# Kernel optimization log

Hardware: AMD Instinct MI355X
Metric: run time of the kernel (lower is better)

The kernel has to match this reference:

```python
import jax, jax.numpy as jnp
import numpy as np

T_TRACK = 256   # tracklets per graph
M_DET = 256     # detections per graph
N_NODES = T_TRACK + M_DET
D_IN = 512      # raw node feature dim (stand-in for CNN crop features)
D_EMB = 256     # node embedding dim
SLACK = 0.2
LAM = 5.0
SINK_ITERS = 8


def box_iou(a, b):
    # a, b: [E,4] boxes (x1,y1,x2,y2)
    ix1 = jnp.maximum(a[:, 0], b[:, 0])
    iy1 = jnp.maximum(a[:, 1], b[:, 1])
    ix2 = jnp.minimum(a[:, 2], b[:, 2])
    iy2 = jnp.minimum(a[:, 3], b[:, 3])
    inter = jnp.clip(ix2 - ix1, 0.0) * jnp.clip(iy2 - iy1, 0.0)
    area_a = (a[:, 2] - a[:, 0]) * (a[:, 3] - a[:, 1])
    area_b = (b[:, 2] - b[:, 0]) * (b[:, 3] - b[:, 1])
    return inter / (area_a + area_b - inter + 1e-8)


def mlp2(x, W1, b1, W2, b2):
    return jax.nn.sigmoid(jax.nn.relu(x @ W1 + b1) @ W2 + b2)


def setup_inputs() -> dict:
    key = jax.random.key(0)
    ks = jax.random.split(key, 16)
    x = jax.random.normal(ks[0], (N_NODES, D_IN), jnp.float32)
    coords = jax.random.uniform(ks[1], (N_NODES, 4), jnp.float32)
    # valid boxes: x1<x2, y1<y2
    c = jax.random.uniform(ks[2], (N_NODES, 2), jnp.float32) * 100.0
    wh = jax.random.uniform(ks[3], (N_NODES, 2), jnp.float32) * 20.0 + 1.0
    coords_original = jnp.concatenate([c, c + wh], axis=1)
    # bipartite edges: track i (node i) <-> det j (node T_TRACK+j), both directions;
    # first T*M edges satisfy src < dst (the half kept by the row<col mask)
    src = jnp.repeat(jnp.arange(T_TRACK, dtype=jnp.int32), M_DET)
    dst = jnp.tile(jnp.arange(M_DET, dtype=jnp.int32) + T_TRACK, T_TRACK)
    edge_index = jnp.stack([jnp.concatenate([src, dst]), jnp.concatenate([dst, src])])
    s = 0.05
    p = lambda k, shp: jax.random.normal(k, shp, jnp.float32) * s
    return dict(
        x=x, coords=coords, coords_original=coords_original, edge_index=edge_index,
        W_cnn=p(ks[4], (D_IN, D_EMB)), b_cnn=jnp.zeros((D_EMB,), jnp.float32),
        Wapp1=p(ks[5], (2 * D_EMB, 128)), bapp1=jnp.zeros((128,), jnp.float32),
        Wapp2=p(ks[6], (128, 1)), bapp2=jnp.zeros((1,), jnp.float32),
        Wg1=p(ks[7], (8, 32)), bg1=jnp.zeros((32,), jnp.float32),
        Wg2=p(ks[8], (32, 1)), bg2=jnp.zeros((1,), jnp.float32),
        Wa1=p(ks[9], (2, 8)), ba1=jnp.zeros((8,), jnp.float32),
        Wa2=p(ks[10], (8, 1)), ba2=jnp.zeros((1,), jnp.float32),
        Wo1=p(ks[11], (D_EMB, D_EMB)), Wo2=p(ks[12], (D_EMB, D_EMB)),
        bo=jnp.zeros((D_EMB,), jnp.float32),
        Wf1=p(ks[13], (2, 8)), bf1=jnp.zeros((8,), jnp.float32),
        Wf2=p(ks[14], (8, 1)), bf2=jnp.zeros((1,), jnp.float32),
    )


def reference(x, coords, coords_original, edge_index, W_cnn, b_cnn, Wapp1, bapp1, Wapp2, bapp2, Wg1, bg1, Wg2, bg2, Wa1, ba1, Wa2, ba2, Wo1, Wo2, bo, Wf1, bf1, Wf2, bf2):
    src, dst = edge_index[0], edge_index[1]
    h = jax.nn.relu(x @ W_cnn + b_cnn)                      # [N, D]
    # per-edge appearance / geometry affinities (vectorized over all edges)
    app = mlp2(jnp.concatenate([h[src], h[dst]], 1), Wapp1, bapp1, Wapp2, bapp2)[:, 0]
    geo = mlp2(jnp.concatenate([coords[src], coords[dst]], 1), Wg1, bg1, Wg2, bg2)[:, 0]
    iou = box_iou(coords_original[src], coords_original[dst])
    e = mlp2(jnp.stack([app, geo], -1), Wa1, ba1, Wa2, ba2)[:, 0]   # [E]
    # message passing (optimNet): edge-gated neighbor aggregation
    agg = jax.ops.segment_sum(e[:, None] * h[src], dst, num_segments=N_NODES)
    out = jax.nn.relu(h @ Wo1 + agg @ Wo2 + bo)             # [N, D]
    # directed (src < dst) half of the edges only
    eh = T_TRACK * M_DET
    a, b = out[src[:eh]], out[dst[:eh]]
    na = jnp.maximum(jnp.linalg.norm(a, axis=-1), 1e-6)
    nb = jnp.maximum(jnp.linalg.norm(b, axis=-1), 1e-6)
    cos = jnp.sum(a * b, -1) / (na * nb)
    score = mlp2(jnp.stack([cos, iou[:eh]], -1), Wf1, bf1, Wf2, bf2)[:, 0]
    # assignment matrix with slack row/col, Sinkhorn normalization
    slack_v = jnp.exp(jnp.float32(LAM * SLACK))
    mat = jnp.full((T_TRACK + 1, M_DET + 1), slack_v, jnp.float32)
    mat = mat.at[:T_TRACK, :M_DET].set(jnp.exp(LAM * score).reshape(T_TRACK, M_DET))
    for _ in range(SINK_ITERS):
        mat = mat / jnp.sum(mat, axis=1, keepdims=True)
        mat = mat / jnp.sum(mat, axis=0, keepdims=True)
    return mat[:T_TRACK, :M_DET].reshape(-1)                # [T*M]
```

## Files before the change

### kernel.cpp

```cpp
#include <hip/hip_runtime.h>
#include <math.h>


__device__ __forceinline__ float sigmoidf_(float x) { return 1.0f / (1.0f + expf(-x)); }

typedef _Float16 h2t __attribute__((ext_vector_type(2)));

__device__ __forceinline__ h2t pack2(float x, float y) {
  h2t r; r.x = (_Float16)x; r.y = (_Float16)y; return r;
}
__device__ __forceinline__ float fdot2f(h2t a, h2t b, float c) {
  return __builtin_amdgcn_fdot2(a, b, c, false);
}
template <int CTRL>
__device__ __forceinline__ float dpp_get(float x) {
  return __builtin_bit_cast(
      float, __builtin_amdgcn_mov_dpp(__builtin_bit_cast(int, x), CTRL, 0xF, 0xF, false));
}
template <int IMM>
__device__ __forceinline__ float swz_get(float x) {
  return __builtin_bit_cast(
      float, __builtin_amdgcn_ds_swizzle(__builtin_bit_cast(int, x), IMM));
}
__device__ __forceinline__ float allred16(float x) {
  x += dpp_get<0xB1>(x);
  x += dpp_get<0x4E>(x);
  x += dpp_get<0x141>(x);
  x += dpp_get<0x140>(x);
  return x;
}

__global__ __launch_bounds__(256)
void k1_h(const float* __restrict__ x, const float* __restrict__ Wc,
          const float* __restrict__ bc, float* __restrict__ h) {
  __shared__ __align__(16) float Ast[2][32][36];
  const int tid = threadIdx.x;
  const int tx = tid & 31, ty = tid >> 5;
  const int ar = tid >> 3, ac = (tid & 7) * 4;
  const int bm = blockIdx.y * 32, bn = blockIdx.x * 32;
  const float* __restrict__ Bp = Wc + bn + tx;
  const float* __restrict__ Ap = x + (bm + ar) * 512 + ac;
  float4 aA, aB;
  float bA[32], bB[32];
  float acc[4] = {0.f, 0.f, 0.f, 0.f};

#define G_LOAD(T, AREG, BARR, AP, BP, LDB)                             \
  {                                                                    \
    AREG = *reinterpret_cast<const float4*>((AP) + (T) * 32);          \
    _Pragma("unroll") for (int kk = 0; kk < 32; ++kk)                  \
        BARR[kk] = (BP)[((T) * 32 + kk) * (LDB)];                      \
  }
#define G_STORE(BUF, AREG)                                             \
  {                                                                    \
    Ast[BUF][ac + 0][ar] = AREG.x; Ast[BUF][ac + 1][ar] = AREG.y;      \
    Ast[BUF][ac + 2][ar] = AREG.z; Ast[BUF][ac + 3][ar] = AREG.w;      \
  }
#define G_COMP(BUF, BARR)                                              \
  {                                                                    \
    _Pragma("unroll") for (int kk = 0; kk < 32; ++kk) {                \
      const float4 a4 =                                                \
          *reinterpret_cast<const float4*>(&Ast[BUF][kk][4 * ty]);     \
      const float bv = BARR[kk];                                       \
      acc[0] = fmaf(a4.x, bv, acc[0]); acc[1] = fmaf(a4.y, bv, acc[1]);\
      acc[2] = fmaf(a4.z, bv, acc[2]); acc[3] = fmaf(a4.w, bv, acc[3]);\
    }                                                                  \
  }

  G_LOAD(0, aA, bA, Ap, Bp, 256);
  G_STORE(0, aA);
  __syncthreads();
  for (int t = 0; t < 16; t += 2) {
    G_LOAD(t + 1, aB, bB, Ap, Bp, 256);
    G_COMP(0, bA);
    G_STORE(1, aB);
    __syncthreads();
    if (t + 2 < 16) { G_LOAD(t + 2, aA, bA, Ap, Bp, 256); }
    G_COMP(1, bB);
    if (t + 2 < 16) { G_STORE(0, aA); }
    __syncthreads();
  }
  const float bias = bc[bn + tx];
#pragma unroll
  for (int i = 0; i < 4; ++i) {
    const float vv = acc[i] + bias;
    h[(bm + 4 * ty + i) * 256 + bn + tx] = vv > 0.f ? vv : 0.f;
  }
}

__global__ __launch_bounds__(256)
void k2_pqgw(const float* __restrict__ h, const float* __restrict__ W1,
             const float* __restrict__ b1, const float* __restrict__ Wo2,
             const float* __restrict__ Wo1, float* __restrict__ PQGW) {
  __shared__ __align__(16) float Ast[2][32][36];
  const int tid = threadIdx.x;
  const int tx = tid & 31, ty = tid >> 5;
  const int ar = tid >> 3, ac = (tid & 7) * 4;
  const int bm = blockIdx.y * 32, bn = blockIdx.x * 32;
  const int col = bn + tx;
  const float* __restrict__ Bp;
  int ldb;
  if (bn < 128)       { Bp = W1 + col; ldb = 128; }
  else if (bn < 256)  { Bp = W1 + 256 * 128 + (col - 128); ldb = 128; }
  else if (bn < 512)  { Bp = Wo2 + (col - 256); ldb = 256; }
  else                { Bp = Wo1 + (col - 512); ldb = 256; }
  const float* __restrict__ Ap = h + (bm + ar) * 256 + ac;
  float4 aA, aB;
  float bA[32], bB[32];
  float acc[4] = {0.f, 0.f, 0.f, 0.f};

  G_LOAD(0, aA, bA, Ap, Bp, ldb);
  G_STORE(0, aA);
  __syncthreads();
  for (int t = 0; t < 8; t += 2) {
    G_LOAD(t + 1, aB, bB, Ap, Bp, ldb);
    G_COMP(0, bA);
    G_STORE(1, aB);
    __syncthreads();
    if (t + 2 < 8) { G_LOAD(t + 2, aA, bA, Ap, Bp, ldb); }
    G_COMP(1, bB);
    if (t + 2 < 8) { G_STORE(0, aA); }
    __syncthreads();
  }
  const float bias = (bn < 128) ? b1[col] : 0.f;
#pragma unroll
  for (int i = 0; i < 4; ++i)
    PQGW[(bm + 4 * ty + i) * 768 + col] = acc[i] + bias;
}

__global__ __launch_bounds__(256)
void k3_edges(const float* __restrict__ PQGW, const float* __restrict__ coords,
              const float* __restrict__ co, const float* __restrict__ Wapp2,
              const float* __restrict__ bapp2, const float* __restrict__ Wg1,
              const float* __restrict__ bg1, const float* __restrict__ Wg2,
              const float* __restrict__ bg2, const float* __restrict__ Wa1,
              const float* __restrict__ ba1, const float* __restrict__ Wa2,
              const float* __restrict__ ba2, float* __restrict__ E1,
              float* __restrict__ E2, float* __restrict__ iou1) {
  __shared__ __align__(16) float Qs[256][33];
  __shared__ __align__(16) float sP[128], sQ[128], sW2[128];
  __shared__ __align__(16) float sWg1[256], sWg2[32], sGfix0[32], sGfix1[32];
  __shared__ float sWa1[16], sBa1[8], sWa2[8];
  const int tid = threadIdx.x;
  const int fr = blockIdx.x;
  if (tid < 128) {
    sP[tid] = PQGW[fr * 768 + tid];
    sQ[tid] = PQGW[fr * 768 + 128 + tid];
    sW2[tid] = Wapp2[tid];
  }
  sWg1[tid] = Wg1[tid];
  if (tid < 32) sWg2[tid] = Wg2[tid];
  if (tid < 16) sWa1[tid] = Wa1[tid];
  if (tid < 8) { sBa1[tid] = ba1[tid]; sWa2[tid] = Wa2[tid]; }
  __syncthreads();
  if (tid < 32) {
    float g0 = bg1[tid], g1 = g0;
#pragma unroll
    for (int q = 0; q < 4; ++q) {
      const float c = coords[fr * 4 + q];
      g0 = fmaf(c, sWg1[q * 32 + tid], g0);
      g1 = fmaf(c, sWg1[(4 + q) * 32 + tid], g1);
    }
    sGfix0[tid] = g0;
    sGfix1[tid] = g1;
  }
  __syncthreads();

  const int d = tid;
  const int srow = tid >> 3, scq = (tid & 7) * 4;
  float z0 = 0.f, z1 = 0.f;
  for (int c8 = 0; c8 < 8; ++c8) {
    const int j0 = c8 * 32;
#pragma unroll
    for (int k = 0; k < 8; ++k) {
      const int r = k * 32 + srow;
      const float4 v = *reinterpret_cast<const float4*>(
          &PQGW[(256 + r) * 768 + j0 + scq]);
      Qs[r][scq + 0] = v.x; Qs[r][scq + 1] = v.y;
      Qs[r][scq + 2] = v.z; Qs[r][scq + 3] = v.w;
    }
    __syncthreads();
    if (j0 < 128) {
#pragma unroll
      for (int j = 0; j < 32; ++j) {
        const int jj = j0 + j;
        float a = sQ[jj] + Qs[d][j];
        a = a > 0.f ? a : 0.f;
        z1 = fmaf(a, sW2[jj], z1);
      }
    } else {
#pragma unroll
      for (int j = 0; j < 32; ++j) {
        const int jj = j0 + j - 128;
        float a = sP[jj] + Qs[d][j];
        a = a > 0.f ? a : 0.f;
        z0 = fmaf(a, sW2[jj], z0);
      }
    }
    __syncthreads();
  }
  const float app0 = sigmoidf_(z0 + bapp2[0]);
  const float app1 = sigmoidf_(z1 + bapp2[0]);
  const float4 cp = *reinterpret_cast<const float4*>(coords + (256 + d) * 4);
  float gz0 = 0.f, gz1 = 0.f;
#pragma unroll
  for (int m = 0; m < 32; ++m) {
    float h0 = sGfix0[m];
    h0 = fmaf(cp.x, sWg1[(4 + 0) * 32 + m], h0);
    h0 = fmaf(cp.y, sWg1[(4 + 1) * 32 + m], h0);
    h0 = fmaf(cp.z, sWg1[(4 + 2) * 32 + m], h0);
    h0 = fmaf(cp.w, sWg1[(4 + 3) * 32 + m], h0);
    h0 = h0 > 0.f ? h0 : 0.f;
    gz0 = fmaf(h0, sWg2[m], gz0);
    float h1 = sGfix1[m];
    h1 = fmaf(cp.x, sWg1[0 * 32 + m], h1);
    h1 = fmaf(cp.y, sWg1[1 * 32 + m], h1);
    h1 = fmaf(cp.z, sWg1[2 * 32 + m], h1);
    h1 = fmaf(cp.w, sWg1[3 * 32 + m], h1);
    h1 = h1 > 0.f ? h1 : 0.f;
    gz1 = fmaf(h1, sWg2[m], gz1);
  }
  const float geo0 = sigmoidf_(gz0 + bg2[0]);
  const float geo1 = sigmoidf_(gz1 + bg2[0]);
  float ez0 = 0.f, ez1 = 0.f;
#pragma unroll
  for (int m = 0; m < 8; ++m) {
    float h0 = fmaf(app0, sWa1[m], fmaf(geo0, sWa1[8 + m], sBa1[m]));
    h0 = h0 > 0.f ? h0 : 0.f;
    ez0 = fmaf(h0, sWa2[m], ez0);
    float h1 = fmaf(app1, sWa1[m], fmaf(geo1, sWa1[8 + m], sBa1[m]));
    h1 = h1 > 0.f ? h1 : 0.f;
    ez1 = fmaf(h1, sWa2[m], ez1);
  }
  E1[fr * 256 + d] = sigmoidf_(ez0 + ba2[0]);
  E2[fr * 256 + d] = sigmoidf_(ez1 + ba2[0]);
  const float4 A4 = *reinterpret_cast<const float4*>(co + fr * 4);
  const float4 B4 = *reinterpret_cast<const float4*>(co + (256 + d) * 4);
  const float ix1 = fmaxf(A4.x, B4.x), iy1 = fmaxf(A4.y, B4.y);
  const float ix2 = fminf(A4.z, B4.z), iy2 = fminf(A4.w, B4.w);
  const float inter = fmaxf(ix2 - ix1, 0.f) * fmaxf(iy2 - iy1, 0.f);
  const float areaA = (A4.z - A4.x) * (A4.w - A4.y);
  const float areaB = (B4.z - B4.x) * (B4.w - B4.y);
  iou1[fr * 256 + d] = inter / (areaA + areaB - inter + 1e-8f);
}

__global__ __launch_bounds__(256)
void k5_out(const float* __restrict__ E1, const float* __restrict__ E2,
            const float* __restrict__ PQGW, const float* __restrict__ bo,
            float* __restrict__ outm) {
  __shared__ __align__(16) float Ast[2][32][36];
  const int tid = threadIdx.x;
  const int tx = tid & 31, ty = tid >> 5;
  const int ar = tid >> 3, ac = (tid & 7) * 4;
  const int bm = blockIdx.y * 32, bn = blockIdx.x * 32;
  const int col = bn + tx;
  const bool detrows = (bm >= 256);
  const float* __restrict__ Ap = detrows
      ? (E1 + ar * 256 + (bm - 256) + ac)
      : (E2 + (bm + ar) * 256 + ac);
  const int astride = detrows ? 256 : 1;
  const float* __restrict__ Bp = PQGW + (detrows ? 0 : 256 * 768) + 256 + col;
  float4 aA, aB;
  float bA[32], bB[32];
  float acc[4] = {0.f, 0.f, 0.f, 0.f};

#define K5_LOAD(T, AREG, BARR)                                         \
  {                                                                    \
    AREG = *reinterpret_cast<const float4*>(Ap + (T) * 32 * astride);  \
    _Pragma("unroll") for (int kk = 0; kk < 32; ++kk)                  \
        BARR[kk] = Bp[((T) * 32 + kk) * 768];                          \
  }
#define K5_STORE(BUF, AREG)                                            \
  {                                                                    \
    if (detrows) {                                                     \
      *reinterpret_cast<float4*>(&Ast[BUF][ar][ac]) = AREG;            \
    } else {                                                           \
      Ast[BUF][ac + 0][ar] = AREG.x; Ast[BUF][ac + 1][ar] = AREG.y;    \
      Ast[BUF][ac + 2][ar] = AREG.z; Ast[BUF][ac + 3][ar] = AREG.w;    \
    }                                                                  \
  }

  K5_LOAD(0, aA, bA);
  K5_STORE(0, aA);
  __syncthreads();
  for (int t = 0; t < 8; t += 2) {
    K5_LOAD(t + 1, aB, bB);
    G_COMP(0, bA);
    K5_STORE(1, aB);
    __syncthreads();
    if (t + 2 < 8) { K5_LOAD(t + 2, aA, bA); }
    G_COMP(1, bB);
    if (t + 2 < 8) { K5_STORE(0, aA); }
    __syncthreads();
  }
  const float bias = bo[col];
#pragma unroll
  for (int i = 0; i < 4; ++i) {
    const float vv = acc[i] + bias + PQGW[(bm + 4 * ty + i) * 768 + 512 + col];
    outm[(bm + 4 * ty + i) * 256 + col] = vv > 0.f ? vv : 0.f;
  }
#undef K5_LOAD
#undef K5_STORE
}

__global__ __launch_bounds__(1024)
void k6_score(const float* __restrict__ outm, const float* __restrict__ iou1,
              const float* __restrict__ Wf1, const float* __restrict__ bf1,
              const float* __restrict__ Wf2, const float* __restrict__ bf2,
              float* __restrict__ Mblk) {
  __shared__ __align__(16) float so[4][260];
  __shared__ __align__(16) float ods[256][33];
  const int tid = threadIdx.x;
  const int team = tid >> 8, d = tid & 255;
  const int s = blockIdx.x * 4 + team;
  so[team][d] = outm[blockIdx.x * 1024 + tid];
  __syncthreads();
  float dot = 0.f, na2 = 0.f, nb2 = 0.f;
  for (int c8 = 0; c8 < 8; ++c8) {
    const int j0 = c8 * 32;
#pragma unroll
    for (int k = 0; k < 2; ++k) {
      const int qi = k * 1024 + tid;
      const int r = qi >> 3, cq = 4 * (qi & 7);
      const float4 v = *reinterpret_cast<const float4*>(
          &outm[(256 + r) * 256 + j0 + cq]);
      ods[r][cq + 0] = v.x; ods[r][cq + 1] = v.y;
      ods[r][cq + 2] = v.z; ods[r][cq + 3] = v.w;
    }
    __syncthreads();
#pragma unroll
    for (int j = 0; j < 32; ++j) {
      const float ov = ods[d][j];
      const float sv = so[team][j0 + j];
      dot = fmaf(sv, ov, dot);
      na2 = fmaf(sv, sv, na2);
      nb2 = fmaf(ov, ov, nb2);
    }
    __syncthreads();
  }
  const float na = fmaxf(sqrtf(na2), 1e-6f);
  const float nb = fmaxf(sqrtf(nb2), 1e-6f);
  const float cosv = dot / (na * nb);
  const float i1 = iou1[s * 256 + d];
  float sz = 0.f;
#pragma unroll
  for (int m = 0; m < 8; ++m) {
    float hm = fmaf(cosv, Wf1[m], fmaf(i1, Wf1[8 + m], bf1[m]));
    hm = hm > 0.f ? hm : 0.f;
    sz = fmaf(hm, Wf2[m], sz);
  }
  const float score = sigmoidf_(sz + bf2[0]);
  Mblk[s * 256 + d] = expf(5.0f * score);
}

__global__ __launch_bounds__(1024)
void k7_sink(const float* __restrict__ Mg, float* __restrict__ outp) {
  __shared__ __align__(16) float su_f[256];
  __shared__ __align__(16) float svs_f[256];
  __shared__ __align__(16) float psum[16][260];
  __shared__ float wsumU[16], wsumV[4];
  const int tid = threadIdx.x, w = tid >> 6, l = tid & 63;
  const float slack = 2.71828182845904523536f;
  const float INV256 = 0.00390625f;
  const int rev = ((l & 1) << 3) | ((l & 2) << 1) | ((l & 4) >> 1) | ((l & 8) >> 3);
  const bool b0 = l & 1, b1 = l & 2, b2 = l & 4, b3 = l & 8;

  h2t mrA[16], mrB[16];
#pragma unroll
  for (int i = 0; i < 16; ++i) {
    const float4 f = *reinterpret_cast<const float4*>(Mg + (w * 16 + i) * 256 + 4 * l);
    mrA[i] = pack2(f.x, f.y);
    mrB[i] = pack2(f.z, f.w);
  }
  if (tid < 256) svs_f[tid] = 256.0f;
  __syncthreads();

  float sv256 = 1.0f;
  for (int it = 0; it < 8; ++it) {
    const float sv_tot =
        (it == 0) ? 257.0f : (wsumV[0] + wsumV[1] + wsumV[2] + wsumV[3] + sv256);
    const float su256 = 1.0f / (slack * sv_tot);
    const float4 va = *reinterpret_cast<const float4*>(&svs_f[4 * l]);
    const h2t sva = pack2(va.x, va.y), svb = pack2(va.z, va.w);
    float p[16];
#pragma unroll
    for (int i = 0; i < 16; ++i) p[i] = fdot2f(mrA[i], sva, fdot2f(mrB[i], svb, 0.0f));
#pragma unroll
    for (int i = 0; i < 8; ++i) {
      const float keep = b0 ? p[i + 8] : p[i], give = b0 ? p[i] : p[i + 8];
      p[i] = keep + dpp_get<0xB1>(give);
    }
#pragma unroll
    for (int i = 0; i < 4; ++i) {
      const float keep = b1 ? p[i + 4] : p[i], give = b1 ? p[i] : p[i + 4];
      p[i] = keep + dpp_get<0x4E>(give);
    }
#pragma unroll
    for (int i = 0; i < 2; ++i) {
      const float keep = b2 ? p[i + 2] : p[i], give = b2 ? p[i] : p[i + 2];
      p[i] = keep + dpp_get<0x141>(give);
    }
    {
      const float keep = b3 ? p[1] : p[0], give = b3 ? p[0] : p[1];
      p[0] = keep + dpp_get<0x140>(give);
    }
    float S = p[0];
    S += swz_get<0x401F>(S);
    S += __shfl_xor(S, 32, 64);
    const float su_val = 1.0f / (S * INV256 + slack * sv256);
    if (l < 16) su_f[w * 16 + rev] = su_val;
    const float wsU = allred16(su_val);
    if (l == 0) wsumU[w] = wsU;
    asm volatile("s_waitcnt lgkmcnt(0)" ::: "memory");
    float su16[16];
#pragma unroll
    for (int k = 0; k < 16; k += 4) {
      const float4 t = *reinterpret_cast<const float4*>(&su_f[w * 16 + k]);
      su16[k] = t.x; su16[k + 1] = t.y; su16[k + 2] = t.z; su16[k + 3] = t.w;
    }
    float pc0 = 0.f, pc1 = 0.f, pc2 = 0.f, pc3 = 0.f;
#pragma unroll
    for (int i = 0; i < 16; ++i) {
      const float ui = su16[i];
      pc0 = fmaf((float)mrA[i].x, ui, pc0);
      pc1 = fmaf((float)mrA[i].y, ui, pc1);
      pc2 = fmaf((float)mrB[i].x, ui, pc2);
      pc3 = fmaf((float)mrB[i].y, ui, pc3);
    }
    float4 pcv; pcv.x = pc0; pcv.y = pc1; pcv.z = pc2; pcv.w = pc3;
    *reinterpret_cast<float4*>(&psum[w][4 * l]) = pcv;
    __syncthreads();
    const float su_tot = wsumU[0] + wsumU[1] + wsumU[2] + wsumU[3] + wsumU[4] +
                         wsumU[5] + wsumU[6] + wsumU[7] + wsumU[8] + wsumU[9] +
                         wsumU[10] + wsumU[11] + wsumU[12] + wsumU[13] +
                         wsumU[14] + wsumU[15] + su256;
    if (tid < 256) {
      float cs = 0.f;
#pragma unroll
      for (int g = 0; g < 16; ++g) cs += psum[g][tid];
      const float sv_val = 1.0f / (cs + slack * su256);
      svs_f[tid] = 256.0f * sv_val;
      float t = allred16(sv_val);
      t += swz_get<0x401F>(t);
      t += __shfl_xor(t, 32, 64);
      if (l == 0) wsumV[w] = t;
    }
    sv256 = 1.0f / (slack * su_tot);
    __syncthreads();
  }
  const float4 sv4 = *reinterpret_cast<const float4*>(&svs_f[4 * l]);
#pragma unroll
  for (int i = 0; i < 16; ++i) {
    const float uo = su_f[w * 16 + i] * INV256;
    float4 o;
    o.x = uo * (float)mrA[i].x * sv4.x;
    o.y = uo * (float)mrA[i].y * sv4.y;
    o.z = uo * (float)mrB[i].x * sv4.z;
    o.w = uo * (float)mrB[i].y * sv4.w;
    *reinterpret_cast<float4*>(outp + (w * 16 + i) * 256 + 4 * l) = o;
  }
}

extern "C" void kernel_launch(void* const* d_in, const int* in_sizes, int n_in,
                              void* d_out, int out_size, void* d_ws, size_t ws_size,
                              hipStream_t stream) {
  (void)in_sizes; (void)n_in; (void)out_size; (void)ws_size;
  const float* x      = (const float*)d_in[0];
  const float* coords = (const float*)d_in[1];
  const float* co     = (const float*)d_in[2];
  const float* Wc    = (const float*)d_in[4];
  const float* bc    = (const float*)d_in[5];
  const float* Wapp1 = (const float*)d_in[6];
  const float* bapp1 = (const float*)d_in[7];
  const float* Wapp2 = (const float*)d_in[8];
  const float* bapp2 = (const float*)d_in[9];
  const float* Wg1   = (const float*)d_in[10];
  const float* bg1   = (const float*)d_in[11];
  const float* Wg2   = (const float*)d_in[12];
  const float* bg2   = (const float*)d_in[13];
  const float* Wa1   = (const float*)d_in[14];
  const float* ba1   = (const float*)d_in[15];
  const float* Wa2   = (const float*)d_in[16];
  const float* ba2   = (const float*)d_in[17];
  const float* Wo1   = (const float*)d_in[18];
  const float* Wo2   = (const float*)d_in[19];
  const float* bo    = (const float*)d_in[20];
  const float* Wf1   = (const float*)d_in[21];
  const float* bf1   = (const float*)d_in[22];
  const float* Wf2   = (const float*)d_in[23];
  const float* bf2   = (const float*)d_in[24];

  float* ws   = (float*)d_ws;
  float* h    = ws + 0;
  float* PQGW = ws + 131072;
  float* E1   = ws + 524288;
  float* E2   = ws + 589824;
  float* iou1 = ws + 655360;
  float* outm = ws + 720896;
  float* Mblk = ws + 851968;

  k1_h<<<dim3(8, 16), 256, 0, stream>>>(x, Wc, bc, h);
  k2_pqgw<<<dim3(24, 16), 256, 0, stream>>>(h, Wapp1, bapp1, Wo2, Wo1, PQGW);
  k3_edges<<<256, 256, 0, stream>>>(PQGW, coords, co, Wapp2, bapp2, Wg1, bg1,
                                    Wg2, bg2, Wa1, ba1, Wa2, ba2, E1, E2, iou1);
  k5_out<<<dim3(8, 16), 256, 0, stream>>>(E1, E2, PQGW, bo, outm);
  k6_score<<<64, 1024, 0, stream>>>(outm, iou1, Wf1, bf1, Wf2, bf2, Mblk);
  k7_sink<<<1, 1024, 0, stream>>>(Mblk, (float*)d_out);
}
```

Baseline: 103.0 us.

## Fuse edge gating with message aggregation per node and tile cosine scoring as GEMM

Merges the edge-MLP kernel and the aggregation GEMM into one kernel with one block per destination node. Each block computes its incoming edge gates into shared memory, immediately reduces them against the neighbour projections, and writes the node output and its L2 norm. The score kernel becomes a tiled 256x256x256 GEMM over track/detection outputs that uses the precomputed norms. This removes one launch and the E1/E2 round trip to global memory, and stops recomputing norms per edge. In exchange, the aggregation reads PQGW columns with a large stride and recomputes the appearance MLP per destination.

```diff
diff --git a/kernel.cpp b/kernel.cpp
--- a/kernel.cpp
+++ b/kernel.cpp
@@ -29,6 +29,28 @@
   x += dpp_get<0x140>(x);
   return x;
 }
+
+#define G_LOAD(T, AREG, BARR, AP, BP, LDB)                             \
+  {                                                                    \
+    AREG = *reinterpret_cast<const float4*>((AP) + (T) * 32);          \
+    _Pragma("unroll") for (int kk = 0; kk < 32; ++kk)                  \
+        BARR[kk] = (BP)[((T) * 32 + kk) * (LDB)];                      \
+  }
+#define G_STORE(BUF, AREG)                                             \
+  {                                                                    \
+    Ast[BUF][ac + 0][ar] = AREG.x; Ast[BUF][ac + 1][ar] = AREG.y;      \
+    Ast[BUF][ac + 2][ar] = AREG.z; Ast[BUF][ac + 3][ar] = AREG.w;      \
+  }
+#define G_COMP(BUF, BARR)                                              \
+  {                                                                    \
+    _Pragma("unroll") for (int kk = 0; kk < 32; ++kk) {                \
+      const float4 a4 =                                                \
+          *reinterpret_cast<const float4*>(&Ast[BUF][kk][4 * ty]);     \
+      const float bv = BARR[kk];                                       \
+      acc[0] = fmaf(a4.x, bv, acc[0]); acc[1] = fmaf(a4.y, bv, acc[1]);\
+      acc[2] = fmaf(a4.z, bv, acc[2]); acc[3] = fmaf(a4.w, bv, acc[3]);\
+    }                                                                  \
+  }
 
 __global__ __launch_bounds__(256)
 void k1_h(const float* __restrict__ x, const float* __restrict__ Wc,
@@ -43,28 +65,6 @@
   float4 aA, aB;
   float bA[32], bB[32];
   float acc[4] = {0.f, 0.f, 0.f, 0.f};
-
-#define G_LOAD(T, AREG, BARR, AP, BP, LDB)                             \
-  {                                                                    \
-    AREG = *reinterpret_cast<const float4*>((AP) + (T) * 32);          \
-    _Pragma("unroll") for (int kk = 0; kk < 32; ++kk)                  \
-        BARR[kk] = (BP)[((T) * 32 + kk) * (LDB)];                      \
-  }
-#define G_STORE(BUF, AREG)                                             \
-  {                                                                    \
-    Ast[BUF][ac + 0][ar] = AREG.x; Ast[BUF][ac + 1][ar] = AREG.y;      \
-    Ast[BUF][ac + 2][ar] = AREG.z; Ast[BUF][ac + 3][ar] = AREG.w;      \
-  }
-#define G_COMP(BUF, BARR)                                              \
-  {                                                                    \
-    _Pragma("unroll") for (int kk = 0; kk < 32; ++kk) {                \
-      const float4 a4 =                                                \
-          *reinterpret_cast<const float4*>(&Ast[BUF][kk][4 * ty]);     \
-      const float bv = BARR[kk];                                       \
-      acc[0] = fmaf(a4.x, bv, acc[0]); acc[1] = fmaf(a4.y, bv, acc[1]);\
-      acc[2] = fmaf(a4.z, bv, acc[2]); acc[3] = fmaf(a4.w, bv, acc[3]);\
-    }                                                                  \
-  }
 
   G_LOAD(0, aA, bA, Ap, Bp, 256);
   G_STORE(0, aA);
@@ -128,23 +128,25 @@
 }
 
 __global__ __launch_bounds__(256)
-void k3_edges(const float* __restrict__ PQGW, const float* __restrict__ coords,
-              const float* __restrict__ co, const float* __restrict__ Wapp2,
-              const float* __restrict__ bapp2, const float* __restrict__ Wg1,
-              const float* __restrict__ bg1, const float* __restrict__ Wg2,
-              const float* __restrict__ bg2, const float* __restrict__ Wa1,
-              const float* __restrict__ ba1, const float* __restrict__ Wa2,
-              const float* __restrict__ ba2, float* __restrict__ E1,
-              float* __restrict__ E2, float* __restrict__ iou1) {
-  __shared__ __align__(16) float Qs[256][33];
-  __shared__ __align__(16) float sP[128], sQ[128], sW2[128];
-  __shared__ __align__(16) float sWg1[256], sWg2[32], sGfix0[32], sGfix1[32];
-  __shared__ float sWa1[16], sBa1[8], sWa2[8];
+void k34_edges_out(const float* __restrict__ PQGW, const float* __restrict__ coords,
+                   const float* __restrict__ co, const float* __restrict__ Wapp2,
+                   const float* __restrict__ bapp2, const float* __restrict__ Wg1,
+                   const float* __restrict__ bg1, const float* __restrict__ Wg2,
+                   const float* __restrict__ bg2, const float* __restrict__ Wa1,
+                   const float* __restrict__ ba1, const float* __restrict__ Wa2,
+                   const float* __restrict__ ba2, const float* __restrict__ bo,
+                   float* __restrict__ iou1, float* __restrict__ outm,
+                   float* __restrict__ nrm) {
+  __shared__ __align__(16) float sQ[128], sW2[128], sWg1[256], sWg2[32], sGfix[32];
+  __shared__ __align__(16) float sE[256];
+  __shared__ float sWa1[16], sBa1[8], sWa2[8], wpart[4];
   const int tid = threadIdx.x;
-  const int fr = blockIdx.x;
+  const int b = blockIdx.x;
+  const bool istrack = (b < 256);
+  const int vbase = istrack ? 256 : 0;
+
   if (tid < 128) {
-    sP[tid] = PQGW[fr * 768 + tid];
-    sQ[tid] = PQGW[fr * 768 + 128 + tid];
+    sQ[tid] = PQGW[b * 768 + 128 + tid];
     sW2[tid] = Wapp2[tid];
   }
   sWg1[tid] = Wg1[tid];
@@ -153,203 +155,138 @@
   if (tid < 8) { sBa1[tid] = ba1[tid]; sWa2[tid] = Wa2[tid]; }
   __syncthreads();
   if (tid < 32) {
-    float g0 = bg1[tid], g1 = g0;
-#pragma unroll
-    for (int q = 0; q < 4; ++q) {
-      const float c = coords[fr * 4 + q];
-      g0 = fmaf(c, sWg1[q * 32 + tid], g0);
-      g1 = fmaf(c, sWg1[(4 + q) * 32 + tid], g1);
-    }
-    sGfix0[tid] = g0;
-    sGfix1[tid] = g1;
-  }
-  __syncthreads();
-
-  const int d = tid;
-  const int srow = tid >> 3, scq = (tid & 7) * 4;
-  float z0 = 0.f, z1 = 0.f;
-  for (int c8 = 0; c8 < 8; ++c8) {
-    const int j0 = c8 * 32;
-#pragma unroll
-    for (int k = 0; k < 8; ++k) {
-      const int r = k * 32 + srow;
-      const float4 v = *reinterpret_cast<const float4*>(
-          &PQGW[(256 + r) * 768 + j0 + scq]);
-      Qs[r][scq + 0] = v.x; Qs[r][scq + 1] = v.y;
-      Qs[r][scq + 2] = v.z; Qs[r][scq + 3] = v.w;
-    }
-    __syncthreads();
-    if (j0 < 128) {
-#pragma unroll
-      for (int j = 0; j < 32; ++j) {
-        const int jj = j0 + j;
-        float a = sQ[jj] + Qs[d][j];
-        a = a > 0.f ? a : 0.f;
-        z1 = fmaf(a, sW2[jj], z1);
-      }
-    } else {
-#pragma unroll
-      for (int j = 0; j < 32; ++j) {
-        const int jj = j0 + j - 128;
-        float a = sP[jj] + Qs[d][j];
-        a = a > 0.f ? a : 0.f;
-        z0 = fmaf(a, sW2[jj], z0);
-      }
-    }
-    __syncthreads();
-  }
-  const float app0 = sigmoidf_(z0 + bapp2[0]);
-  const float app1 = sigmoidf_(z1 + bapp2[0]);
-  const float4 cp = *reinterpret_cast<const float4*>(coords + (256 + d) * 4);
-  float gz0 = 0.f, gz1 = 0.f;
+    float g = bg1[tid];
+#pragma unroll
+    for (int q = 0; q < 4; ++q)
+      g = fmaf(coords[b * 4 + q], sWg1[(4 + q) * 32 + tid], g);
+    sGfix[tid] = g;
+  }
+  __syncthreads();
+
+  const int vr = vbase + tid;
+  const float* prow = PQGW + vr * 768;
+  float z = 0.f;
+#pragma unroll
+  for (int j = 0; j < 128; j += 4) {
+    const float4 p4 = *reinterpret_cast<const float4*>(prow + j);
+    const float4 q4 = *reinterpret_cast<const float4*>(&sQ[j]);
+    const float4 w4 = *reinterpret_cast<const float4*>(&sW2[j]);
+    float a;
+    a = p4.x + q4.x; a = a > 0.f ? a : 0.f; z = fmaf(a, w4.x, z);
+    a = p4.y + q4.y; a = a > 0.f ? a : 0.f; z = fmaf(a, w4.y, z);
+    a = p4.z + q4.z; a = a > 0.f ? a : 0.f; z = fmaf(a, w4.z, z);
+    a = p4.w + q4.w; a = a > 0.f ? a : 0.f; z = fmaf(a, w4.w, z);
+  }
+  const float app = sigmoidf_(z + bapp2[0]);
+  const float4 cp = *reinterpret_cast<const float4*>(coords + vr * 4);
+  float gz = 0.f;
 #pragma unroll
   for (int m = 0; m < 32; ++m) {
-    float h0 = sGfix0[m];
-    h0 = fmaf(cp.x, sWg1[(4 + 0) * 32 + m], h0);
-    h0 = fmaf(cp.y, sWg1[(4 + 1) * 32 + m], h0);
-    h0 = fmaf(cp.z, sWg1[(4 + 2) * 32 + m], h0);
-    h0 = fmaf(cp.w, sWg1[(4 + 3) * 32 + m], h0);
-    h0 = h0 > 0.f ? h0 : 0.f;
-    gz0 = fmaf(h0, sWg2[m], gz0);
-    float h1 = sGfix1[m];
-    h1 = fmaf(cp.x, sWg1[0 * 32 + m], h1);
-    h1 = fmaf(cp.y, sWg1[1 * 32 + m], h1);
-    h1 = fmaf(cp.z, sWg1[2 * 32 + m], h1);
-    h1 = fmaf(cp.w, sWg1[3 * 32 + m], h1);
-    h1 = h1 > 0.f ? h1 : 0.f;
-    gz1 = fmaf(h1, sWg2[m], gz1);
-  }
-  const float geo0 = sigmoidf_(gz0 + bg2[0]);
-  const float geo1 = sigmoidf_(gz1 + bg2[0]);
-  float ez0 = 0.f, ez1 = 0.f;
+    float hm = sGfix[m];
+    hm = fmaf(cp.x, sWg1[0 * 32 + m], hm);
+    hm = fmaf(cp.y, sWg1[1 * 32 + m], hm);
+    hm = fmaf(cp.z, sWg1[2 * 32 + m], hm);
+    hm = fmaf(cp.w, sWg1[3 * 32 + m], hm);
+    hm = hm > 0.f ? hm : 0.f;
+    gz = fmaf(hm, sWg2[m], gz);
+  }
+  const float geo = sigmoidf_(gz + bg2[0]);
+  float ez = 0.f;
 #pragma unroll
   for (int m = 0; m < 8; ++m) {
-    float h0 = fmaf(app0, sWa1[m], fmaf(geo0, sWa1[8 + m], sBa1[m]));
-    h0 = h0 > 0.f ? h0 : 0.f;
-    ez0 = fmaf(h0, sWa2[m], ez0);
-    float h1 = fmaf(app1, sWa1[m], fmaf(geo1, sWa1[8 + m], sBa1[m]));
-    h1 = h1 > 0.f ? h1 : 0.f;
-    ez1 = fmaf(h1, sWa2[m], ez1);
-  }
-  E1[fr * 256 + d] = sigmoidf_(ez0 + ba2[0]);
-  E2[fr * 256 + d] = sigmoidf_(ez1 + ba2[0]);
-  const float4 A4 = *reinterpret_cast<const float4*>(co + fr * 4);
-  const float4 B4 = *reinterpret_cast<const float4*>(co + (256 + d) * 4);
-  const float ix1 = fmaxf(A4.x, B4.x), iy1 = fmaxf(A4.y, B4.y);
-  const float ix2 = fminf(A4.z, B4.z), iy2 = fminf(A4.w, B4.w);
-  const float inter = fmaxf(ix2 - ix1, 0.f) * fmaxf(iy2 - iy1, 0.f);
-  const float areaA = (A4.z - A4.x) * (A4.w - A4.y);
-  const float areaB = (B4.z - B4.x) * (B4.w - B4.y);
-  iou1[fr * 256 + d] = inter / (areaA + areaB - inter + 1e-8f);
+    float hm = fmaf(app, sWa1[m], fmaf(geo, sWa1[8 + m], sBa1[m]));
+    hm = hm > 0.f ? hm : 0.f;
+    ez = fmaf(hm, sWa2[m], ez);
+  }
+  sE[tid] = sigmoidf_(ez + ba2[0]);
+  if (istrack) {
+    const float4 A4 = *reinterpret_cast<const float4*>(co + b * 4);
+    const float4 B4 = *reinterpret_cast<const float4*>(co + (256 + tid) * 4);
+    const float ix1 = fmaxf(A4.x, B4.x), iy1 = fmaxf(A4.y, B4.y);
+    const float ix2 = fminf(A4.z, B4.z), iy2 = fminf(A4.w, B4.w);
+    const float inter = fmaxf(ix2 - ix1, 0.f) * fmaxf(iy2 - iy1, 0.f);
+    const float areaA = (A4.z - A4.x) * (A4.w - A4.y);
+    const float areaB = (B4.z - B4.x) * (B4.w - B4.y);
+    iou1[b * 256 + tid] = inter / (areaA + areaB - inter + 1e-8f);
+  }
+  __syncthreads();
+
+  const int c = tid;
+  float a0 = 0.f, a1 = 0.f, a2 = 0.f, a3 = 0.f;
+  const float* gcol = PQGW + vbase * 768 + 256 + c;
+#pragma unroll 4
+  for (int j = 0; j < 256; j += 4) {
+    const float4 e4 = *reinterpret_cast<const float4*>(&sE[j]);
+    a0 = fmaf(e4.x, gcol[(j + 0) * 768], a0);
+    a1 = fmaf(e4.y, gcol[(j + 1) * 768], a1);
+    a2 = fmaf(e4.z, gcol[(j + 2) * 768], a2);
+    a3 = fmaf(e4.w, gcol[(j + 3) * 768], a3);
+  }
+  const float base = PQGW[b * 768 + 512 + c] + bo[c];
+  float vv = base + ((a0 + a1) + (a2 + a3));
+  vv = vv > 0.f ? vv : 0.f;
+  outm[b * 256 + c] = vv;
+  float nsq = vv * vv;
+  nsq = allred16(nsq);
+  nsq += swz_get<0x401F>(nsq);
+  nsq += __shfl_xor(nsq, 32, 64);
+  if ((tid & 63) == 0) wpart[tid >> 6] = nsq;
+  __syncthreads();
+  if (tid == 0)
+    nrm[b] = fmaxf(sqrtf(wpart[0] + wpart[1] + wpart[2] + wpart[3]), 1e-6f);
 }
 
 __global__ __launch_bounds__(256)
-void k5_out(const float* __restrict__ E1, const float* __restrict__ E2,
-            const float* __restrict__ PQGW, const float* __restrict__ bo,
-            float* __restrict__ outm) {
+void k6_score(const float* __restrict__ outm, const float* __restrict__ nrm,
+              const float* __restrict__ iou1, const float* __restrict__ Wf1,
+              const float* __restrict__ bf1, const float* __restrict__ Wf2,
+              const float* __restrict__ bf2, float* __restrict__ Mblk) {
   __shared__ __align__(16) float Ast[2][32][36];
   const int tid = threadIdx.x;
   const int tx = tid & 31, ty = tid >> 5;
   const int ar = tid >> 3, ac = (tid & 7) * 4;
-  const int bm = blockIdx.y * 32, bn = blockIdx.x * 32;
-  const int col = bn + tx;
-  const bool detrows = (bm >= 256);
-  const float* __restrict__ Ap = detrows
-      ? (E1 + ar * 256 + (bm - 256) + ac)
-      : (E2 + (bm + ar) * 256 + ac);
-  const int astride = detrows ? 256 : 1;
-  const float* __restrict__ Bp = PQGW + (detrows ? 0 : 256 * 768) + 256 + col;
+  const int s0 = blockIdx.y * 32, d0 = blockIdx.x * 32;
+  const float* __restrict__ Ap = outm + (s0 + ar) * 256 + ac;
+  const float* __restrict__ Bp = outm + (256 + d0 + tx) * 256;
   float4 aA, aB;
   float bA[32], bB[32];
   float acc[4] = {0.f, 0.f, 0.f, 0.f};
 
-#define K5_LOAD(T, AREG, BARR)                                         \
-  {                                                                    \
-    AREG = *reinterpret_cast<const float4*>(Ap + (T) * 32 * astride);  \
-    _Pragma("unroll") for (int kk = 0; kk < 32; ++kk)                  \
-        BARR[kk] = Bp[((T) * 32 + kk) * 768];                          \
-  }
-#define K5_STORE(BUF, AREG)                                            \
-  {                                                                    \
-    if (detrows) {                                                     \
-      *reinterpret_cast<float4*>(&Ast[BUF][ar][ac]) = AREG;            \
-    } else {                                                           \
-      Ast[BUF][ac + 0][ar] = AREG.x; Ast[BUF][ac + 1][ar] = AREG.y;    \
-      Ast[BUF][ac + 2][ar] = AREG.z; Ast[BUF][ac + 3][ar] = AREG.w;    \
-    }                                                                  \
-  }
-
-  K5_LOAD(0, aA, bA);
-  K5_STORE(0, aA);
+  G_LOAD(0, aA, bA, Ap, Bp, 1);
+  G_STORE(0, aA);
   __syncthreads();
   for (int t = 0; t < 8; t += 2) {
-    K5_LOAD(t + 1, aB, bB);
+    G_LOAD(t + 1, aB, bB, Ap, Bp, 1);
     G_COMP(0, bA);
-    K5_STORE(1, aB);
-    __syncthreads();
-    if (t + 2 < 8) { K5_LOAD(t + 2, aA, bA); }
+    G_STORE(1, aB);
+    __syncthreads();
+    if (t + 2 < 8) { G_LOAD(t + 2, aA, bA, Ap, Bp, 1); }
     G_COMP(1, bB);
-    if (t + 2 < 8) { K5_STORE(0, aA); }
-    __syncthreads();
-  }
-  const float bias = bo[col];
+    if (t + 2 < 8) { G_STORE(0, aA); }
+    __syncthreads();
+  }
+  const float nb = nrm[256 + d0 + tx];
+  float w1c[8], w1i[8], w2[8];
+#pragma unroll
+  for (int m = 0; m < 8; ++m) {
+    w1c[m] = Wf1[m]; w1i[m] = Wf1[8 + m]; w2[m] = Wf2[m];
+  }
+  const float bf20 = bf2[0];
 #pragma unroll
   for (int i = 0; i < 4; ++i) {
-    const float vv = acc[i] + bias + PQGW[(bm + 4 * ty + i) * 768 + 512 + col];
-    outm[(bm + 4 * ty + i) * 256 + col] = vv > 0.f ? vv : 0.f;
-  }
-#undef K5_LOAD
-#undef K5_STORE
-}
-
-__global__ __launch_bounds__(1024)
-void k6_score(const float* __restrict__ outm, const float* __restrict__ iou1,
-              const float* __restrict__ Wf1, const float* __restrict__ bf1,
-              const float* __restrict__ Wf2, const float* __restrict__ bf2,
-              float* __restrict__ Mblk) {
-  __shared__ __align__(16) float so[4][260];
-  __shared__ __align__(16) float ods[256][33];
-  const int tid = threadIdx.x;
-  const int team = tid >> 8, d = tid & 255;
-  const int s = blockIdx.x * 4 + team;
-  so[team][d] = outm[blockIdx.x * 1024 + tid];
-  __syncthreads();
-  float dot = 0.f, na2 = 0.f, nb2 = 0.f;
-  for (int c8 = 0; c8 < 8; ++c8) {
-    const int j0 = c8 * 32;
-#pragma unroll
-    for (int k = 0; k < 2; ++k) {
-      const int qi = k * 1024 + tid;
-      const int r = qi >> 3, cq = 4 * (qi & 7);
-      const float4 v = *reinterpret_cast<const float4*>(
-          &outm[(256 + r) * 256 + j0 + cq]);
-      ods[r][cq + 0] = v.x; ods[r][cq + 1] = v.y;
-      ods[r][cq + 2] = v.z; ods[r][cq + 3] = v.w;
-    }
-    __syncthreads();
-#pragma unroll
-    for (int j = 0; j < 32; ++j) {
-      const float ov = ods[d][j];
-      const float sv = so[team][j0 + j];
-      dot = fmaf(sv, ov, dot);
-      na2 = fmaf(sv, sv, na2);
-      nb2 = fmaf(ov, ov, nb2);
-    }
-    __syncthreads();
-  }
-  const float na = fmaxf(sqrtf(na2), 1e-6f);
-  const float nb = fmaxf(sqrtf(nb2), 1e-6f);
-  const float cosv = dot / (na * nb);
-  const float i1 = iou1[s * 256 + d];
-  float sz = 0.f;
-#pragma unroll
-  for (int m = 0; m < 8; ++m) {
-    float hm = fmaf(cosv, Wf1[m], fmaf(i1, Wf1[8 + m], bf1[m]));
-    hm = hm > 0.f ? hm : 0.f;
-    sz = fmaf(hm, Wf2[m], sz);
-  }
-  const float score = sigmoidf_(sz + bf2[0]);
-  Mblk[s * 256 + d] = expf(5.0f * score);
+    const int r = s0 + 4 * ty + i;
+    const float cosv = acc[i] / (nrm[r] * nb);
+    const float i1 = iou1[r * 256 + d0 + tx];
+    float sz = 0.f;
+#pragma unroll
+    for (int m = 0; m < 8; ++m) {
+      float hm = fmaf(cosv, w1c[m], fmaf(i1, w1i[m], bf1[m]));
+      hm = hm > 0.f ? hm : 0.f;
+      sz = fmaf(hm, w2[m], sz);
+    }
+    const float score = sigmoidf_(sz + bf20);
+    Mblk[r * 256 + d0 + tx] = expf(5.0f * score);
+  }
 }
 
 __global__ __launch_bounds__(1024)
@@ -492,17 +429,17 @@
   float* ws   = (float*)d_ws;
   float* h    = ws + 0;
   float* PQGW = ws + 131072;
-  float* E1   = ws + 524288;
-  float* E2   = ws + 589824;
-  float* iou1 = ws + 655360;
-  float* outm = ws + 720896;
-  float* Mblk = ws + 851968;
+  float* iou1 = ws + 524288;
+  float* outm = ws + 589824;
+  float* nrm  = ws + 720896;
+  float* Mblk = ws + 721408;
 
   k1_h<<<dim3(8, 16), 256, 0, stream>>>(x, Wc, bc, h);
   k2_pqgw<<<dim3(24, 16), 256, 0, stream>>>(h, Wapp1, bapp1, Wo2, Wo1, PQGW);
-  k3_edges<<<256, 256, 0, stream>>>(PQGW, coords, co, Wapp2, bapp2, Wg1, bg1,
-                                    Wg2, bg2, Wa1, ba1, Wa2, ba2, E1, E2, iou1);
-  k5_out<<<dim3(8, 16), 256, 0, stream>>>(E1, E2, PQGW, bo, outm);
-  k6_score<<<64, 1024, 0, stream>>>(outm, iou1, Wf1, bf1, Wf2, bf2, Mblk);
+  k34_edges_out<<<512, 256, 0, stream>>>(PQGW, coords, co, Wapp2, bapp2, Wg1,
+                                         bg1, Wg2, bg2, Wa1, ba1, Wa2, ba2, bo,
+                                         iou1, outm, nrm);
+  k6_score<<<dim3(8, 8), 256, 0, stream>>>(outm, nrm, iou1, Wf1, bf1, Wf2, bf2,
+                                           Mblk);
   k7_sink<<<1, 1024, 0, stream>>>(Mblk, (float*)d_out);
 }
```

Result: faster. 95.95 us (-6.9%).
